# Kernel optimization log

Measured on AMD Instinct MI355X. Metric: run time of the kernel, lower is better.

Reference implementation:

```python
import jax, jax.numpy as jnp
import numpy as np

OUT_FEATURES = 11008
IN_FEATURES = 4096
PACKED_LEN = OUT_FEATURES * IN_FEATURES // 4  # 4 ternary vals per byte, 2 bits each


def setup_inputs() -> dict:
    key = jax.random.key(0)
    k1, k2, k3 = jax.random.split(key, 3)
    x = jax.random.normal(k1, (4, 1024, IN_FEATURES), dtype=jnp.float32)
    packed_weight = jax.random.randint(k2, (PACKED_LEN,), 0, 256, dtype=jnp.int32)
    weight_scale = jax.random.uniform(k3, (1,), dtype=jnp.float32)
    return {"x": x, "packed_weight": packed_weight, "weight_scale": weight_scale}


def _dequantize_weight(packed_weight, weight_scale):
    shifts = jnp.arange(0, 8, 2, dtype=jnp.int32)          # [4]
    q = ((packed_weight[:, None] >> shifts) & 3) - 1        # [P, 4]
    q = q.reshape(OUT_FEATURES, IN_FEATURES).astype(jnp.float32)
    return q * weight_scale.reshape(())                      # dequantize


def reference(x, packed_weight, weight_scale):
    w = _dequantize_weight(packed_weight, weight_scale)      # [out, in]
    # F.linear: y = x @ w.T  (bias=False)
    return jnp.einsum('bsi,oi->bso', x, w)
```

## Files before the change

kernel.cpp:

```cpp
#include <hip/hip_runtime.h>
#include <hip/hip_bf16.h>

#define OUT_F 11008
#define IN_F  4096
#define M_DIM 4096

typedef __attribute__((ext_vector_type(8))) short bf16x8;
typedef __attribute__((ext_vector_type(4))) float f32x4;
typedef __attribute__((ext_vector_type(8))) unsigned short us8;

__device__ __forceinline__ unsigned short f2bf_rne(float f) {
    unsigned u = __builtin_bit_cast(unsigned, f);
    u += 0x7fffu + ((u >> 16) & 1u);
    return (unsigned short)(u >> 16);
}

__global__ void prep_kernel(const float* __restrict__ x,
                            unsigned short* __restrict__ xb,
                            const int* __restrict__ pw,
                            unsigned short* __restrict__ wb) {
    if (blockIdx.x < 8192) {
        size_t i = ((size_t)blockIdx.x * blockDim.x + threadIdx.x) * 8;
        float4 a = *(const float4*)(x + i);
        float4 b = *(const float4*)(x + i + 4);
        us8 o;
        o[0] = f2bf_rne(a.x); o[1] = f2bf_rne(a.y);
        o[2] = f2bf_rne(a.z); o[3] = f2bf_rne(a.w);
        o[4] = f2bf_rne(b.x); o[5] = f2bf_rne(b.y);
        o[6] = f2bf_rne(b.z); o[7] = f2bf_rne(b.w);
        *(us8*)(xb + i) = o;
    } else {
        size_t i = ((size_t)(blockIdx.x - 8192)) * blockDim.x + threadIdx.x;
        int4 v = ((const int4*)pw)[i];
        const unsigned long long LUT = 0x40003F800000BF80ull;
        us8 o0, o1;
#pragma unroll
        for (int j = 0; j < 4; j++) {
            o0[j]     = (unsigned short)(LUT >> (((v.x >> (2 * j)) & 3) * 16));
            o0[4 + j] = (unsigned short)(LUT >> (((v.y >> (2 * j)) & 3) * 16));
            o1[j]     = (unsigned short)(LUT >> (((v.z >> (2 * j)) & 3) * 16));
            o1[4 + j] = (unsigned short)(LUT >> (((v.w >> (2 * j)) & 3) * 16));
        }
        ((us8*)wb)[i * 2]     = o0;
        ((us8*)wb)[i * 2 + 1] = o1;
    }
}

__global__ __launch_bounds__(512, 2) void gemm_kernel(
    const unsigned short* __restrict__ A,
    const unsigned short* __restrict__ B,
    float* __restrict__ C,
    const float* __restrict__ scale_ptr) {
    constexpr int K  = IN_F;
    constexpr int N  = OUT_F;
    constexpr int NT = K / 64;

    __shared__ unsigned short lds[2][2][2][256][32];

    const int tid  = threadIdx.x;
    const int wave = tid >> 6;
    const int lane = tid & 63;
    const int quad = lane >> 4;
    const int mrow = lane & 15;
    const int sw   = quad ^ ((mrow >> 1) & 3);

    const int srow = lane >> 2;
    const int sseg = (lane & 3) ^ ((lane >> 3) & 3);

    const int lin = blockIdx.x;
    const int xcd = lin & 7;
    const int q   = lin >> 3;
    const int bm  = xcd * 2 + q / 43;
    const int bn  = q % 43;

    const int wm = (wave >> 2) * 128;
    const int wn = (wave & 3) * 64;

    const unsigned short* Ag = A + (size_t)bm * 256 * K;
    const unsigned short* Bg = B + (size_t)bn * 256 * K;

    f32x4 acc[8][4];
#pragma unroll
    for (int i = 0; i < 8; i++)
#pragma unroll
        for (int j = 0; j < 4; j++) acc[i][j] = (f32x4){0.f, 0.f, 0.f, 0.f};

    auto STAGE = [&](int mat, int nb, int h, int kbase) {
#pragma unroll
        for (int c = 0; c < 2; ++c) {
            const int chunk = wave * 2 + c;
            const int grow  = chunk * 16 + srow;
            const unsigned short* src =
                (mat ? Bg : Ag) + (size_t)grow * K + kbase + sseg * 8;
            __builtin_amdgcn_global_load_lds(
                (const __attribute__((address_space(1))) void*)src,
                (__attribute__((address_space(3))) void*)
                    (&lds[nb][mat][h][0][0] + chunk * 512),
                16, 0, 0);
        }
    };

    STAGE(0, 0, 0, 0);
    STAGE(1, 0, 0, 0);
    STAGE(0, 0, 1, 32);
    STAGE(1, 0, 1, 32);
    __syncthreads();

    for (int kt = 0; kt < NT; ++kt) {
        const int  buf  = kt & 1;
        const int  nbuf = buf ^ 1;
        const bool pf   = (kt + 1 < NT);
        const int  kn   = (kt + 1) * 64;

        if (pf) {
            STAGE(0, nbuf, 0, kn);
            STAGE(1, nbuf, 0, kn);
            STAGE(0, nbuf, 1, kn + 32);
            STAGE(1, nbuf, 1, kn + 32);
        }

#pragma unroll
        for (int h = 0; h < 2; ++h) {
            bf16x8 a[8], b[4];
#pragma unroll
            for (int t = 0; t < 8; ++t)
                a[t] = *(const bf16x8*)&lds[buf][0][h][wm + t * 16 + mrow][sw * 8];
#pragma unroll
            for (int j = 0; j < 4; ++j)
                b[j] = *(const bf16x8*)&lds[buf][1][h][wn + j * 16 + mrow][sw * 8];
#pragma unroll
            for (int t = 0; t < 8; ++t)
#pragma unroll
                for (int j = 0; j < 4; ++j)
                    acc[t][j] = __builtin_amdgcn_mfma_f32_16x16x32_bf16(
                        a[t], b[j], acc[t][j], 0, 0, 0);
        }

        __syncthreads();
    }

    const float scale = *scale_ptr;
    float* Cg = C + (size_t)(bm * 256 + wm) * N + bn * 256 + wn;
#pragma unroll
    for (int i = 0; i < 8; ++i) {
#pragma unroll
        for (int j = 0; j < 4; ++j) {
#pragma unroll
            for (int r = 0; r < 4; ++r) {
                const int row = i * 16 + quad * 4 + r;
                const int col = j * 16 + mrow;
                Cg[(size_t)row * N + col] = acc[i][j][r] * scale;
            }
        }
    }
}

extern "C" void kernel_launch(void* const* d_in, const int* in_sizes, int n_in,
                              void* d_out, int out_size, void* d_ws, size_t ws_size,
                              hipStream_t stream) {
    const float* x   = (const float*)d_in[0];
    const int* pw    = (const int*)d_in[1];
    const float* wsc = (const float*)d_in[2];

    float* out = (float*)d_out;

    unsigned short* xb = (unsigned short*)d_ws;
    unsigned short* wb = (unsigned short*)((char*)d_ws + (size_t)M_DIM * IN_F * 2);

    prep_kernel<<<8192 + 11008, 256, 0, stream>>>(x, xb, pw, wb);

    gemm_kernel<<<688, 512, 0, stream>>>(xb, wb, out, wsc);
}
```

Measured before the change: 603.0 us.

## Software-pipeline LDS fragment loads with MFMAs and split per-iteration barriers

Restructures the GEMM main loop so LDS fragment reads for the next quarter-tile are issued while MFMAs on the current fragments run, and the first fragments of the next k-tile are prefetched before the loop-end barrier. The single __syncthreads is replaced by an explicit vmcnt(0) wait plus s_barrier in mid-iteration and a bare s_barrier at the end. This aims to hide LDS read latency behind matrix-core work. It raises register pressure and depends on getting the hand-placed waits right.

```diff
diff --git a/kernel.cpp b/kernel.cpp
--- a/kernel.cpp
+++ b/kernel.cpp
@@ -46,6 +46,9 @@
     }
 }
 
+#define VMCNT(n) do { asm volatile("s_waitcnt vmcnt(" #n ")" ::: "memory"); \
+                      __builtin_amdgcn_sched_barrier(0); } while (0)
+
 __global__ __launch_bounds__(512, 2) void gemm_kernel(
     const unsigned short* __restrict__ A,
     const unsigned short* __restrict__ B,
@@ -104,7 +107,16 @@
     STAGE(1, 0, 0, 0);
     STAGE(0, 0, 1, 32);
     STAGE(1, 0, 1, 32);
-    __syncthreads();
+    VMCNT(0);
+    __builtin_amdgcn_s_barrier();
+
+    bf16x8 aC[4], aN[4], bA[4], bB[4];
+#pragma unroll
+    for (int t = 0; t < 4; ++t)
+        aC[t] = *(const bf16x8*)&lds[0][0][0][wm + t * 16 + mrow][sw * 8];
+#pragma unroll
+    for (int j = 0; j < 4; ++j)
+        bA[j] = *(const bf16x8*)&lds[0][1][0][wn + j * 16 + mrow][sw * 8];
 
     for (int kt = 0; kt < NT; ++kt) {
         const int  buf  = kt & 1;
@@ -112,6 +124,13 @@
         const bool pf   = (kt + 1 < NT);
         const int  kn   = (kt + 1) * 64;
 
+#pragma unroll
+        for (int t = 0; t < 4; ++t)
+            aN[t] = *(const bf16x8*)&lds[buf][0][0][wm + 64 + t * 16 + mrow][sw * 8];
+#pragma unroll
+        for (int j = 0; j < 4; ++j)
+            bB[j] = *(const bf16x8*)&lds[buf][1][1][wn + j * 16 + mrow][sw * 8];
+
         if (pf) {
             STAGE(0, nbuf, 0, kn);
             STAGE(1, nbuf, 0, kn);
@@ -120,23 +139,54 @@
         }
 
 #pragma unroll
-        for (int h = 0; h < 2; ++h) {
-            bf16x8 a[8], b[4];
-#pragma unroll
-            for (int t = 0; t < 8; ++t)
-                a[t] = *(const bf16x8*)&lds[buf][0][h][wm + t * 16 + mrow][sw * 8];
-#pragma unroll
-            for (int j = 0; j < 4; ++j)
-                b[j] = *(const bf16x8*)&lds[buf][1][h][wn + j * 16 + mrow][sw * 8];
-#pragma unroll
-            for (int t = 0; t < 8; ++t)
-#pragma unroll
-                for (int j = 0; j < 4; ++j)
-                    acc[t][j] = __builtin_amdgcn_mfma_f32_16x16x32_bf16(
-                        a[t], b[j], acc[t][j], 0, 0, 0);
-        }
-
-        __syncthreads();
+        for (int t = 0; t < 4; ++t)
+#pragma unroll
+            for (int j = 0; j < 4; ++j)
+                acc[t][j] = __builtin_amdgcn_mfma_f32_16x16x32_bf16(
+                    aC[t], bA[j], acc[t][j], 0, 0, 0);
+
+#pragma unroll
+        for (int t = 0; t < 4; ++t)
+            aC[t] = *(const bf16x8*)&lds[buf][0][1][wm + t * 16 + mrow][sw * 8];
+
+#pragma unroll
+        for (int t = 0; t < 4; ++t)
+#pragma unroll
+            for (int j = 0; j < 4; ++j)
+                acc[4 + t][j] = __builtin_amdgcn_mfma_f32_16x16x32_bf16(
+                    aN[t], bA[j], acc[4 + t][j], 0, 0, 0);
+
+        VMCNT(0);
+        __builtin_amdgcn_s_barrier();
+
+#pragma unroll
+        for (int t = 0; t < 4; ++t)
+            aN[t] = *(const bf16x8*)&lds[buf][0][1][wm + 64 + t * 16 + mrow][sw * 8];
+
+#pragma unroll
+        for (int t = 0; t < 4; ++t)
+#pragma unroll
+            for (int j = 0; j < 4; ++j)
+                acc[t][j] = __builtin_amdgcn_mfma_f32_16x16x32_bf16(
+                    aC[t], bB[j], acc[t][j], 0, 0, 0);
+
+        if (pf) {
+#pragma unroll
+            for (int t = 0; t < 4; ++t)
+                aC[t] = *(const bf16x8*)&lds[nbuf][0][0][wm + t * 16 + mrow][sw * 8];
+#pragma unroll
+            for (int j = 0; j < 4; ++j)
+                bA[j] = *(const bf16x8*)&lds[nbuf][1][0][wn + j * 16 + mrow][sw * 8];
+        }
+
+#pragma unroll
+        for (int t = 0; t < 4; ++t)
+#pragma unroll
+            for (int j = 0; j < 4; ++j)
+                acc[4 + t][j] = __builtin_amdgcn_mfma_f32_16x16x32_bf16(
+                    aN[t], bB[j], acc[4 + t][j], 0, 0, 0);
+
+        __builtin_amdgcn_s_barrier();
     }
 
     const float scale = *scale_ptr;
```

Result: slower. 642.9 us (+6.6%).

## Keep weights packed as 2-bit and unpack into LDS inside the GEMM

Applied to the files above, without the earlier changes.

The prep kernel now compacts the int32-per-byte packed weights into real bytes, in a K-tile-major layout, instead of expanding them to a full bf16 matrix. The GEMM stages these packed bytes into LDS two tiles ahead and unpacks them to bf16 with byte-permute instructions into a swizzled LDS B tile. This removes the large bf16 weight write and re-read from global memory. In exchange the GEMM main loop gains ALU and LDS-store work plus a deeper pipeline, which may compete with the MFMA work.

```diff
diff --git a/kernel.cpp b/kernel.cpp
--- a/kernel.cpp
+++ b/kernel.cpp
@@ -18,7 +18,7 @@
 __global__ void prep_kernel(const float* __restrict__ x,
                             unsigned short* __restrict__ xb,
                             const int* __restrict__ pw,
-                            unsigned short* __restrict__ wb) {
+                            unsigned char* __restrict__ pw2) {
     if (blockIdx.x < 8192) {
         size_t i = ((size_t)blockIdx.x * blockDim.x + threadIdx.x) * 8;
         float4 a = *(const float4*)(x + i);
@@ -30,32 +30,47 @@
         o[6] = f2bf_rne(b.z); o[7] = f2bf_rne(b.w);
         *(us8*)(xb + i) = o;
     } else {
-        size_t i = ((size_t)(blockIdx.x - 8192)) * blockDim.x + threadIdx.x;
-        int4 v = ((const int4*)pw)[i];
-        const unsigned long long LUT = 0x40003F800000BF80ull;
-        us8 o0, o1;
-#pragma unroll
-        for (int j = 0; j < 4; j++) {
-            o0[j]     = (unsigned short)(LUT >> (((v.x >> (2 * j)) & 3) * 16));
-            o0[4 + j] = (unsigned short)(LUT >> (((v.y >> (2 * j)) & 3) * 16));
-            o1[j]     = (unsigned short)(LUT >> (((v.z >> (2 * j)) & 3) * 16));
-            o1[4 + j] = (unsigned short)(LUT >> (((v.w >> (2 * j)) & 3) * 16));
-        }
-        ((us8*)wb)[i * 2]     = o0;
-        ((us8*)wb)[i * 2 + 1] = o1;
+        const int kb   = blockIdx.x - 8192;
+        const int kt   = kb & 63;
+        const int rgrp = kb >> 6;
+        const int row  = rgrp * 256 + threadIdx.x;
+        const int4* src = (const int4*)(pw + (size_t)row * 1024 + kt * 16);
+        unsigned out[4];
+#pragma unroll
+        for (int i = 0; i < 4; ++i) {
+            int4 v = src[i];
+            out[i] = (v.x & 0xFF) | ((v.y & 0xFF) << 8) |
+                     ((v.z & 0xFF) << 16) | ((unsigned)v.w << 24);
+        }
+        *(uint4*)(pw2 + ((size_t)kt * OUT_F + row) * 16) =
+            *(const uint4*)out;
     }
+}
+
+__device__ __forceinline__ void unpack_byte(unsigned b, unsigned& d_lo,
+                                            unsigned& d_hi) {
+    const unsigned PA = 0x00800080u;
+    const unsigned PB = 0x403F00BFu;
+    unsigned m0 = (b & 0xFu) * 0x00404101u;
+    unsigned s0 = (m0 & 0x03030303u) | 0x00040004u;
+    d_lo = __builtin_amdgcn_perm(PA, PB, s0);
+    unsigned m1 = (b >> 4) * 0x00404101u;
+    unsigned s1 = (m1 & 0x03030303u) | 0x00040004u;
+    d_hi = __builtin_amdgcn_perm(PA, PB, s1);
 }
 
 __global__ __launch_bounds__(512, 2) void gemm_kernel(
     const unsigned short* __restrict__ A,
-    const unsigned short* __restrict__ B,
+    const unsigned char* __restrict__ P,
     float* __restrict__ C,
     const float* __restrict__ scale_ptr) {
     constexpr int K  = IN_F;
     constexpr int N  = OUT_F;
     constexpr int NT = K / 64;
 
-    __shared__ unsigned short lds[2][2][2][256][32];
+    __shared__ unsigned short sA[2][2][256][32];
+    __shared__ unsigned short sB[2][2][256][32];
+    __shared__ unsigned char  pb[2][4096];
 
     const int tid  = threadIdx.x;
     const int wave = tid >> 6;
@@ -77,7 +92,6 @@
     const int wn = (wave & 3) * 64;
 
     const unsigned short* Ag = A + (size_t)bm * 256 * K;
-    const unsigned short* Bg = B + (size_t)bn * 256 * K;
 
     f32x4 acc[8][4];
 #pragma unroll
@@ -85,49 +99,77 @@
 #pragma unroll
         for (int j = 0; j < 4; j++) acc[i][j] = (f32x4){0.f, 0.f, 0.f, 0.f};
 
-    auto STAGE = [&](int mat, int nb, int h, int kbase) {
-#pragma unroll
-        for (int c = 0; c < 2; ++c) {
-            const int chunk = wave * 2 + c;
-            const int grow  = chunk * 16 + srow;
-            const unsigned short* src =
-                (mat ? Bg : Ag) + (size_t)grow * K + kbase + sseg * 8;
+    auto STAGE_A = [&](int nb, int kbase) {
+#pragma unroll
+        for (int h = 0; h < 2; ++h) {
+#pragma unroll
+            for (int c = 0; c < 2; ++c) {
+                const int chunk = wave * 2 + c;
+                const int grow  = chunk * 16 + srow;
+                const unsigned short* src =
+                    Ag + (size_t)grow * K + kbase + h * 32 + sseg * 8;
+                __builtin_amdgcn_global_load_lds(
+                    (const __attribute__((address_space(1))) void*)src,
+                    (__attribute__((address_space(3))) void*)
+                        (&sA[nb][h][0][0] + chunk * 512),
+                    16, 0, 0);
+            }
+        }
+    };
+    auto STAGE_P = [&](int nb, int kt) {
+        if (wave < 4) {
+            const unsigned char* src =
+                P + ((size_t)kt * N + bn * 256 + wave * 64 + lane) * 16;
             __builtin_amdgcn_global_load_lds(
                 (const __attribute__((address_space(1))) void*)src,
-                (__attribute__((address_space(3))) void*)
-                    (&lds[nb][mat][h][0][0] + chunk * 512),
+                (__attribute__((address_space(3))) void*)(&pb[nb][wave * 1024]),
                 16, 0, 0);
         }
     };
-
-    STAGE(0, 0, 0, 0);
-    STAGE(1, 0, 0, 0);
-    STAGE(0, 0, 1, 32);
-    STAGE(1, 0, 1, 32);
+    auto UNPACK = [&](int srcb, int dstb) {
+        const int row = tid >> 1;
+        const int h   = tid & 1;
+        unsigned long long pk =
+            *(const unsigned long long*)&pb[srcb][tid * 8];
+        const int rsw = (row >> 1) & 3;
+#pragma unroll
+        for (int s = 0; s < 4; ++s) {
+            unsigned p16 = (unsigned)(pk >> (16 * s)) & 0xFFFFu;
+            unsigned d0, d1, d2, d3;
+            unpack_byte(p16 & 0xFFu, d0, d1);
+            unpack_byte(p16 >> 8, d2, d3);
+            const int slot = s ^ rsw;
+            *(uint4*)&sB[dstb][h][row][slot * 8] = (uint4){d0, d1, d2, d3};
+        }
+    };
+
+    STAGE_A(0, 0);
+    STAGE_P(1, 0);
+    __syncthreads();
+    UNPACK(1, 0);
+    STAGE_P(0, 1);
     __syncthreads();
 
     for (int kt = 0; kt < NT; ++kt) {
         const int  buf  = kt & 1;
         const int  nbuf = buf ^ 1;
-        const bool pf   = (kt + 1 < NT);
-        const int  kn   = (kt + 1) * 64;
-
-        if (pf) {
-            STAGE(0, nbuf, 0, kn);
-            STAGE(1, nbuf, 0, kn);
-            STAGE(0, nbuf, 1, kn + 32);
-            STAGE(1, nbuf, 1, kn + 32);
-        }
+        const bool pf1  = (kt + 1 < NT);
+        const bool pf2  = (kt + 2 < NT);
+
+        if (pf1) STAGE_A(nbuf, (kt + 1) * 64);
+        if (pf2) STAGE_P(nbuf, kt + 2);
+
+        if (pf1) UNPACK(buf, nbuf);
 
 #pragma unroll
         for (int h = 0; h < 2; ++h) {
             bf16x8 a[8], b[4];
 #pragma unroll
             for (int t = 0; t < 8; ++t)
-                a[t] = *(const bf16x8*)&lds[buf][0][h][wm + t * 16 + mrow][sw * 8];
+                a[t] = *(const bf16x8*)&sA[buf][h][wm + t * 16 + mrow][sw * 8];
 #pragma unroll
             for (int j = 0; j < 4; ++j)
-                b[j] = *(const bf16x8*)&lds[buf][1][h][wn + j * 16 + mrow][sw * 8];
+                b[j] = *(const bf16x8*)&sB[buf][h][wn + j * 16 + mrow][sw * 8];
 #pragma unroll
             for (int t = 0; t < 8; ++t)
 #pragma unroll
@@ -164,10 +206,11 @@
 
     float* out = (float*)d_out;
 
-    unsigned short* xb = (unsigned short*)d_ws;
-    unsigned short* wb = (unsigned short*)((char*)d_ws + (size_t)M_DIM * IN_F * 2);
-
-    prep_kernel<<<8192 + 11008, 256, 0, stream>>>(x, xb, pw, wb);
-
-    gemm_kernel<<<688, 512, 0, stream>>>(xb, wb, out, wsc);
-}
+    unsigned short* xb  = (unsigned short*)d_ws;
+    unsigned char*  pw2 = (unsigned char*)((char*)d_ws
+                          + (size_t)M_DIM * IN_F * 2);
+
+    prep_kernel<<<8192 + 2752, 256, 0, stream>>>(x, xb, pw, pw2);
+
+    gemm_kernel<<<688, 512, 0, stream>>>(xb, pw2, out, wsc);
+}
```

Result: slower. 620.1 us (+2.8%).
